# Kernel optimization log

Measured on AMD Instinct MI355X. Metric: run time of the kernel, lower is better.

The kernel has to match this reference:

```python
import jax, jax.numpy as jnp
import numpy as np

B, T, P, D, H = 16, 512, 576, 1024, 16
HD = D // H  # head_dim = 64
SCALE = 1.0 / np.sqrt(HD).astype(np.float32)


def _split_heads(x):
    # [B, S, D] -> [B, H, S, HD]
    b, s, _ = x.shape
    return x.reshape(b, s, H, HD).transpose(0, 2, 1, 3)


def _merge_heads(x):
    # [B, H, S, HD] -> [B, S, D]
    b, h, s, hd = x.shape
    return x.transpose(0, 2, 1, 3).reshape(b, s, h * hd)


def _linear(x, w, b):
    # torch nn.Linear: y = x @ W^T + b, W is [out, in]
    return jnp.einsum('bsd,od->bso', x, w) + b


def setup_inputs() -> dict:
    key = jax.random.key(0)
    ks = jax.random.split(key, 12)
    inp = {
        'text_feats': jax.random.normal(ks[0], (B, T, D), jnp.float32),
        'image_feats': jax.random.normal(ks[1], (B, P, D), jnp.float32),
        'text_mask': jnp.ones((B, T), dtype=bool),
    }
    names = ['qt', 'ki', 'vi', 'qi', 'kt', 'vt', 'ot', 'oi']
    for i, n in enumerate(names):
        inp['w_' + n] = jax.random.normal(ks[2 + i], (D, D), jnp.float32) * 0.02
        inp['b_' + n] = jnp.zeros((D,), jnp.float32)
    return inp


def reference(text_feats, image_feats, text_mask,
              w_qt, b_qt, w_ki, b_ki, w_vi, b_vi,
              w_qi, b_qi, w_kt, b_kt, w_vt, b_vt,
              w_ot, b_ot, w_oi, b_oi):
    # ---- text attends to image (no mask on image keys) ----
    q_t = _split_heads(_linear(text_feats, w_qt, b_qt))    # [B,H,T,HD]
    k_i = _split_heads(_linear(image_feats, w_ki, b_ki))   # [B,H,P,HD]
    v_i = _split_heads(_linear(image_feats, w_vi, b_vi))   # [B,H,P,HD]
    scores_ti = jnp.einsum('bhtd,bhpd->bhtp', q_t, k_i) * SCALE
    attn_ti = jax.nn.softmax(scores_ti, axis=-1)
    text_attended = _merge_heads(jnp.einsum('bhtp,bhpd->bhtd', attn_ti, v_i))
    text_attended = _linear(text_attended, w_ot, b_ot)

    # ---- image attends to text (mask on text keys) ----
    q_i = _split_heads(_linear(image_feats, w_qi, b_qi))   # [B,H,P,HD]
    k_t = _split_heads(_linear(text_feats, w_kt, b_kt))    # [B,H,T,HD]
    v_t = _split_heads(_linear(text_feats, w_vt, b_vt))    # [B,H,T,HD]
    scores_it = jnp.einsum('bhpd,bhtd->bhpt', q_i, k_t) * SCALE
    scores_it = jnp.where(text_mask[:, None, None, :], scores_it, -jnp.inf)
    attn_it = jax.nn.softmax(scores_it, axis=-1)
    image_attended = _merge_heads(jnp.einsum('bhpt,bhtd->bhpd', attn_it, v_t))
    image_attended = _linear(image_attended, w_oi, b_oi)

    return (text_attended, image_attended)
```

## Files before the change

### kernel.cpp

```cpp
#include <hip/hip_runtime.h>
#include <stdint.h>

typedef unsigned short u16;
typedef __bf16 bf16x8 __attribute__((ext_vector_type(8)));
typedef float f32x4 __attribute__((ext_vector_type(4)));

#define SCALE_QK 0.125f

__device__ __forceinline__ u16 f2bf(float f) {
    uint32_t u = __builtin_bit_cast(uint32_t, f);
    u += 0x7FFFu + ((u >> 16) & 1u);
    return (u16)(u >> 16);
}

__device__ __forceinline__ int bdiv(int x, int S) {
    return (S == 512) ? (x >> 9) : (int)(((uint64_t)(x >> 6) * 954437177ull) >> 33);
}

__global__ void cvt_f32_bf16(const float* __restrict__ src, u16* __restrict__ dst, int n4) {
    int i = blockIdx.x * blockDim.x + threadIdx.x;
    if (i >= n4) return;
    float4 v = ((const float4*)src)[i];
    ushort4 o;
    o.x = f2bf(v.x); o.y = f2bf(v.y); o.z = f2bf(v.z); o.w = f2bf(v.w);
    ((ushort4*)dst)[i] = o;
}

__global__ void mask_prep(const int* __restrict__ maski, float* __restrict__ mb, int n) {
    int i = blockIdx.x * blockDim.x + threadIdx.x;
    if (i >= n) return;
    int v0 = maski[0];
    int v = (v0 == 0x01010101) ? (int)((const unsigned char*)maski)[i] : maski[i];
    mb[i] = v ? 0.0f : -1e30f;
}

__device__ __forceinline__ void gload_lds16(const void* g, void* l) {
    __builtin_amdgcn_global_load_lds(
        (__attribute__((address_space(1))) void*)(g),
        (__attribute__((address_space(3))) void*)(l), 16, 0, 0);
}

template<int LAYOUT>
__global__ __launch_bounds__(256)
void gemm_bt(const u16* __restrict__ A, const u16* __restrict__ Bt,
             const float* __restrict__ bias, void* __restrict__ Cout,
             int nx, int K, int ldc, int S, size_t partStride) {
    __shared__ u16 As[128 * 32];
    __shared__ u16 Bs[128 * 32];
    const int tid = threadIdx.x;
    const int wid = tid >> 6, lane = tid & 63;
    const int lo = lane & 15, hi = lane >> 4;
    const int wr = wid >> 1, wc = wid & 1;
    const int id = blockIdx.x;
    const int f = (id & 7) * ((int)gridDim.x >> 3) + (id >> 3);
    const int bm = f / nx, bn = f - bm * nx;
    const u16* Ab = A + (size_t)bm * 128 * K;
    const u16* Bb = Bt + (size_t)bn * 128 * K;
    f32x4 acc[4][4] = {};
    for (int k0 = 0; k0 < K; k0 += 32) {
#pragma unroll
        for (int it = 0; it < 2; ++it) {
            int eo = it * 2048 + wid * 512 + lane * 8;
            int row = eo >> 5, kk = eo & 31;
            gload_lds16(Ab + (size_t)row * K + k0 + kk, As + it * 2048 + wid * 512);
            gload_lds16(Bb + (size_t)row * K + k0 + kk, Bs + it * 2048 + wid * 512);
        }
        __syncthreads();
        bf16x8 af[4], bfr[4];
        const int koff = hi * 8;
#pragma unroll
        for (int m = 0; m < 4; ++m)
            af[m] = *(const bf16x8*)(As + (wr * 64 + m * 16 + lo) * 32 + koff);
#pragma unroll
        for (int n = 0; n < 4; ++n)
            bfr[n] = *(const bf16x8*)(Bs + (wc * 64 + n * 16 + lo) * 32 + koff);
        __builtin_amdgcn_s_setprio(1);
#pragma unroll
        for (int m = 0; m < 4; ++m)
#pragma unroll
            for (int n = 0; n < 4; ++n)
                acc[m][n] = __builtin_amdgcn_mfma_f32_16x16x32_bf16(af[m], bfr[n], acc[m][n], 0, 0, 0);
        __builtin_amdgcn_s_setprio(0);
        __syncthreads();
    }
    const int rowbase = bm * 128 + wr * 64, colbase = bn * 128 + wc * 64;

    if (LAYOUT == 0) {
        float* C = (float*)Cout;
#pragma unroll
        for (int m = 0; m < 4; ++m)
#pragma unroll
            for (int r = 0; r < 4; ++r) {
                int row = rowbase + m * 16 + hi * 4 + r;
#pragma unroll
                for (int n = 0; n < 4; ++n) {
                    int col = colbase + n * 16 + lo;
                    C[(size_t)row * ldc + col] = acc[m][n][r] + bias[col];
                }
            }
    } else if (LAYOUT == 1) {
        const int part = colbase >> 10;
        const int h = (colbase >> 6) & 15;
        u16* base = (u16*)Cout + (size_t)part * partStride;
        float bv[4];
#pragma unroll
        for (int n = 0; n < 4; ++n) bv[n] = bias[colbase + n * 16 + lo];
#pragma unroll
        for (int m = 0; m < 4; ++m)
#pragma unroll
            for (int r = 0; r < 4; ++r) {
                int row = rowbase + m * 16 + hi * 4 + r;
                int b = bdiv(row, S);
                int s = row - b * S;
                u16* rp = base + (((size_t)(b * 16 + h) * S + s) << 6);
#pragma unroll
                for (int n = 0; n < 4; ++n)
                    rp[n * 16 + lo] = f2bf(acc[m][n][r] + bv[n]);
            }
    } else {
        u16* base = (u16*)Cout;
        int bn_[4], s0_[4];
#pragma unroll
        for (int n = 0; n < 4; ++n) {
            int col0 = colbase + n * 16;
            int b = bdiv(col0, S);
            bn_[n] = b;
            s0_[n] = col0 - b * S;
        }
#pragma unroll
        for (int m = 0; m < 4; ++m)
#pragma unroll
            for (int r = 0; r < 4; ++r) {
                int dout = rowbase + m * 16 + hi * 4 + r;
                float bv = bias[dout];
                size_t hd = (size_t)(dout >> 6) * 64 + (dout & 63);
#pragma unroll
                for (int n = 0; n < 4; ++n)
                    base[((size_t)(bn_[n] * 16) * 64 + hd) * S + s0_[n] + lo] =
                        f2bf(acc[m][n][r] + bv);
            }
    }
}

template<int MASKED, int NQ, int SK>
__global__ __launch_bounds__(256)
void attn_v4(const u16* __restrict__ Q, const u16* __restrict__ Kb,
             const u16* __restrict__ Vt, const float* __restrict__ mb,
             u16* __restrict__ Out) {
    constexpr int SQ = NQ * 64;
    constexpr int NC = SK / 64;
    __shared__ u16 kls[2][64 * 64];
    __shared__ u16 vls[2][64 * 64];
    __shared__ u16 pls[4][16 * 72];
    const int tid = threadIdx.x, wid = tid >> 6, lane = tid & 63;
    const int lo = lane & 15, hi = lane >> 4;
    const int id = blockIdx.x;
    const int f = (id & 7) * (NQ * 32) + (id >> 3);
    const int qc = f % NQ, bh = f / NQ;
    const int b = bh >> 4, h = bh & 15;
    const int q0 = qc * 64 + wid * 16;
    const u16* Qp = Q + ((size_t)bh * SQ + q0) * 64;
    const u16* Kp = Kb + (size_t)bh * SK * 64;
    const u16* Vp = Vt + (size_t)bh * 64 * SK;

    bf16x8 qf[2];
#pragma unroll
    for (int ks = 0; ks < 2; ++ks)
        qf[ks] = *(const bf16x8*)(Qp + lo * 64 + ks * 32 + hi * 8);

    f32x4 oacc[4] = {};
    float m = -3e38f, l = 0.f;
    u16* pl = pls[wid];
    uint32_t* pl32 = (uint32_t*)pl;

    auto stage = [&](int bufi, int c0) {
#pragma unroll
        for (int j = 0; j < 2; ++j) {
            const int beta = (j * 4 + wid) * 64 + lane;
            const int row = beta >> 3, slot = beta & 7;
            const int e = (slot ^ (row & 7)) << 3;
            gload_lds16(Kp + (size_t)(c0 + row) * 64 + e,
                        &kls[bufi][0] + (j * 4 + wid) * 512);
            gload_lds16(Vp + (size_t)row * SK + c0 + e,
                        &vls[bufi][0] + (j * 4 + wid) * 512);
        }
    };

    stage(0, 0);
    __syncthreads();

    for (int c = 0; c < NC; ++c) {
        const int c0 = c * 64;
        if (c + 1 < NC) stage((c + 1) & 1, c0 + 64);
        const u16* kb = &kls[c & 1][0];
        const u16* vb = &vls[c & 1][0];

        float sc[4][4];
#pragma unroll
        for (int kt = 0; kt < 4; ++kt) {
            const int krow = kt * 16 + lo;
            const int rx = krow & 7;
            bf16x8 kf0 = *(const bf16x8*)(kb + krow * 64 + ((hi ^ rx) << 3));
            bf16x8 kf1 = *(const bf16x8*)(kb + krow * 64 + (((4 + hi) ^ rx) << 3));
            f32x4 z = {};
            __builtin_amdgcn_s_setprio(1);
            z = __builtin_amdgcn_mfma_f32_16x16x32_bf16(kf0, qf[0], z, 0, 0, 0);
            z = __builtin_amdgcn_mfma_f32_16x16x32_bf16(kf1, qf[1], z, 0, 0, 0);
            __builtin_amdgcn_s_setprio(0);
            if (MASKED) {
                float4 mv = *(const float4*)(mb + b * SK + c0 + kt * 16 + hi * 4);
#pragma unroll
                for (int r = 0; r < 4; ++r) sc[kt][r] = z[r] * SCALE_QK + ((const float*)&mv)[r];
            } else {
#pragma unroll
                for (int r = 0; r < 4; ++r) sc[kt][r] = z[r] * SCALE_QK;
            }
        }
        float a0 = fmaxf(fmaxf(sc[0][0], sc[0][1]), fmaxf(sc[0][2], sc[0][3]));
        float a1 = fmaxf(fmaxf(sc[1][0], sc[1][1]), fmaxf(sc[1][2], sc[1][3]));
        float a2 = fmaxf(fmaxf(sc[2][0], sc[2][1]), fmaxf(sc[2][2], sc[2][3]));
        float a3 = fmaxf(fmaxf(sc[3][0], sc[3][1]), fmaxf(sc[3][2], sc[3][3]));
        float pmax = fmaxf(fmaxf(a0, a1), fmaxf(a2, a3));
        pmax = fmaxf(pmax, __shfl_xor(pmax, 16));
        pmax = fmaxf(pmax, __shfl_xor(pmax, 32));
        if (!__all(pmax - m <= 8.0f)) {
            float mn = fmaxf(m, pmax);
            float alpha = __expf(m - mn);
            m = mn;
            l *= alpha;
#pragma unroll
            for (int n = 0; n < 4; ++n)
#pragma unroll
                for (int r = 0; r < 4; ++r) oacc[n][r] *= alpha;
        }
        float sum = 0.f;
#pragma unroll
        for (int kt = 0; kt < 4; ++kt) {
#pragma unroll
            for (int r = 0; r < 4; ++r) {
                float p = __expf(sc[kt][r] - m);
                sc[kt][r] = p;
                sum += p;
            }
        }
        sum += __shfl_xor(sum, 16);
        sum += __shfl_xor(sum, 32);
        l += sum;
#pragma unroll
        for (int kt = 0; kt < 4; ++kt) {
#pragma unroll
            for (int rp = 0; rp < 2; ++rp) {
                uint32_t w = (uint32_t)f2bf(sc[kt][2 * rp]) |
                             ((uint32_t)f2bf(sc[kt][2 * rp + 1]) << 16);
                pl32[lo * 36 + kt * 8 + hi * 2 + rp] = w;
            }
        }
        bf16x8 pf0 = *(const bf16x8*)(pl + lo * 72 + hi * 8);
        bf16x8 pf1 = *(const bf16x8*)(pl + lo * 72 + 32 + hi * 8);
        __builtin_amdgcn_s_setprio(1);
#pragma unroll
        for (int n = 0; n < 4; ++n) {
            const int d = n * 16 + lo;
            const int dx = d & 7;
            bf16x8 v0 = *(const bf16x8*)(vb + d * 64 + ((hi ^ dx) << 3));
            bf16x8 v1 = *(const bf16x8*)(vb + d * 64 + (((4 + hi) ^ dx) << 3));
            oacc[n] = __builtin_amdgcn_mfma_f32_16x16x32_bf16(v0, pf0, oacc[n], 0, 0, 0);
            oacc[n] = __builtin_amdgcn_mfma_f32_16x16x32_bf16(v1, pf1, oacc[n], 0, 0, 0);
        }
        __builtin_amdgcn_s_setprio(0);
        __syncthreads();
    }
    const float inv = 1.0f / l;
    u16* op = Out + ((size_t)(b * SQ + q0 + lo)) * 1024 + h * 64;
#pragma unroll
    for (int n = 0; n < 4; ++n) {
        ushort4 w;
        w.x = f2bf(oacc[n][0] * inv);
        w.y = f2bf(oacc[n][1] * inv);
        w.z = f2bf(oacc[n][2] * inv);
        w.w = f2bf(oacc[n][3] * inv);
        *(ushort4*)(op + n * 16 + hi * 4) = w;
    }
}

extern "C" void kernel_launch(void* const* d_in, const int* in_sizes, int n_in,
                              void* d_out, int out_size, void* d_ws, size_t ws_size,
                              hipStream_t stream) {
    (void)in_sizes; (void)n_in; (void)out_size; (void)ws_size;
    const float* text  = (const float*)d_in[0];
    const float* image = (const float*)d_in[1];
    const int*   maski = (const int*)d_in[2];
    const float* w_qt = (const float*)d_in[3];  const float* b_qt = (const float*)d_in[4];
    const float* w_ki = (const float*)d_in[5];  const float* b_ki = (const float*)d_in[6];
    const float* w_vi = (const float*)d_in[7];  const float* b_vi = (const float*)d_in[8];
    const float* w_qi = (const float*)d_in[9];  const float* b_qi = (const float*)d_in[10];
    const float* w_kt = (const float*)d_in[11]; const float* b_kt = (const float*)d_in[12];
    const float* w_vt = (const float*)d_in[13]; const float* b_vt = (const float*)d_in[14];
    const float* w_ot = (const float*)d_in[15]; const float* b_ot = (const float*)d_in[16];
    const float* w_oi = (const float*)d_in[17]; const float* b_oi = (const float*)d_in[18];

    const int B = 16, T = 512, P = 576, D = 1024;
    const int MT = B * T;
    const int MI = B * P;

    char* wp = (char*)d_ws;
    auto alloc = [&](size_t bytes) { char* r = wp; wp += (bytes + 255) & ~(size_t)255; return r; };
    u16* Xt    = (u16*)alloc((size_t)MT * D * 2);
    u16* Xi    = (u16*)alloc((size_t)MI * D * 2);
    u16* Wqk_t = (u16*)alloc((size_t)2 * D * D * 2);
    u16* Wqk_i = (u16*)alloc((size_t)2 * D * D * 2);
    u16* Wv_t  = (u16*)alloc((size_t)D * D * 2);
    u16* Wv_i  = (u16*)alloc((size_t)D * D * 2);
    u16* Wot   = (u16*)alloc((size_t)D * D * 2);
    u16* Woi   = (u16*)alloc((size_t)D * D * 2);
    float* bqk_t = (float*)alloc((size_t)2 * D * 4);
    float* bqk_i = (float*)alloc((size_t)2 * D * 4);
    float* mbf   = (float*)alloc((size_t)B * T * 4);
    u16* QKt  = (u16*)alloc((size_t)2 * MT * D * 2);
    u16* QKi  = (u16*)alloc((size_t)2 * MI * D * 2);
    u16* Vtt  = (u16*)alloc((size_t)MT * D * 2);
    u16* Vti  = (u16*)alloc((size_t)MI * D * 2);

    auto cvt = [&](const float* s, u16* d, size_t n) {
        int n4 = (int)(n / 4);
        cvt_f32_bf16<<<(n4 + 255) / 256, 256, 0, stream>>>(s, d, n4);
    };
    cvt(text, Xt, (size_t)MT * D);
    cvt(image, Xi, (size_t)MI * D);
    cvt(w_qt, Wqk_t,                 (size_t)D * D);
    cvt(w_kt, Wqk_t + (size_t)D * D, (size_t)D * D);
    cvt(w_qi, Wqk_i,                 (size_t)D * D);
    cvt(w_ki, Wqk_i + (size_t)D * D, (size_t)D * D);
    cvt(w_vt, Wv_t, (size_t)D * D);
    cvt(w_vi, Wv_i, (size_t)D * D);
    cvt(w_ot, Wot,  (size_t)D * D);
    cvt(w_oi, Woi,  (size_t)D * D);
    hipMemcpyAsync(bqk_t,     b_qt, D * 4, hipMemcpyDeviceToDevice, stream);
    hipMemcpyAsync(bqk_t + D, b_kt, D * 4, hipMemcpyDeviceToDevice, stream);
    hipMemcpyAsync(bqk_i,     b_qi, D * 4, hipMemcpyDeviceToDevice, stream);
    hipMemcpyAsync(bqk_i + D, b_ki, D * 4, hipMemcpyDeviceToDevice, stream);
    mask_prep<<<(B * T + 255) / 256, 256, 0, stream>>>(maski, mbf, B * T);

    gemm_bt<1><<<(2 * D / 128) * (MT / 128), 256, 0, stream>>>(
        Xt, Wqk_t, bqk_t, QKt, 2 * D / 128, D, 0, T, (size_t)MT * D);
    gemm_bt<1><<<(2 * D / 128) * (MI / 128), 256, 0, stream>>>(
        Xi, Wqk_i, bqk_i, QKi, 2 * D / 128, D, 0, P, (size_t)MI * D);
    gemm_bt<2><<<(MT / 128) * (D / 128), 256, 0, stream>>>(
        Wv_t, Xt, b_vt, Vtt, MT / 128, D, 0, T, 0);
    gemm_bt<2><<<(MI / 128) * (D / 128), 256, 0, stream>>>(
        Wv_i, Xi, b_vi, Vti, MI / 128, D, 0, P, 0);

    attn_v4<0, 8, 576><<<8 * 256, 256, 0, stream>>>(
        QKt, QKi + (size_t)MI * D, Vti, nullptr, Xt);
    attn_v4<1, 9, 512><<<9 * 256, 256, 0, stream>>>(
        QKi, QKt + (size_t)MT * D, Vtt, mbf, Xi);

    gemm_bt<0><<<(D / 128) * (MT / 128), 256, 0, stream>>>(
        Xt, Wot, b_ot, d_out, D / 128, D, D, T, 0);
    gemm_bt<0><<<(D / 128) * (MI / 128), 256, 0, stream>>>(
        Xi, Woi, b_oi, (void*)((float*)d_out + (size_t)MT * D), D / 128, D, D, P, 0);
}
```

Measured before the change: 394.7 us.

## Replace GEMMs with 256x256 double-buffered tiles and batch paired launches

```diff
diff --git a/kernel.cpp b/kernel.cpp
--- a/kernel.cpp
+++ b/kernel.cpp
@@ -15,6 +15,12 @@
 
 __device__ __forceinline__ int bdiv(int x, int S) {
     return (S == 512) ? (x >> 9) : (int)(((uint64_t)(x >> 6) * 954437177ull) >> 33);
+}
+
+__device__ __forceinline__ void gload_lds16(const void* g, void* l) {
+    __builtin_amdgcn_global_load_lds(
+        (__attribute__((address_space(1))) void*)(g),
+        (__attribute__((address_space(3))) void*)(l), 16, 0, 0);
 }
 
 __global__ void cvt_f32_bf16(const float* __restrict__ src, u16* __restrict__ dst, int n4) {
@@ -26,99 +32,159 @@
     ((ushort4*)dst)[i] = o;
 }
 
-__global__ void mask_prep(const int* __restrict__ maski, float* __restrict__ mb, int n) {
+struct Ptr8 { const float* p[8]; };
+
+__global__ void cvt_w8(Ptr8 srcs, u16* __restrict__ dst) {
     int i = blockIdx.x * blockDim.x + threadIdx.x;
-    if (i >= n) return;
-    int v0 = maski[0];
-    int v = (v0 == 0x01010101) ? (int)((const unsigned char*)maski)[i] : maski[i];
-    mb[i] = v ? 0.0f : -1e30f;
-}
-
-__device__ __forceinline__ void gload_lds16(const void* g, void* l) {
-    __builtin_amdgcn_global_load_lds(
-        (__attribute__((address_space(1))) void*)(g),
-        (__attribute__((address_space(3))) void*)(l), 16, 0, 0);
+    int mat = i >> 18, off = i & 262143;
+    float4 v = ((const float4*)srcs.p[mat])[off];
+    ushort4 o;
+    o.x = f2bf(v.x); o.y = f2bf(v.y); o.z = f2bf(v.z); o.w = f2bf(v.w);
+    ((ushort4*)(dst + ((size_t)mat << 20)))[off] = o;
+}
+
+__global__ void prep(const int* __restrict__ maski, float* __restrict__ mb,
+                     const float* __restrict__ bqt, const float* __restrict__ bkt,
+                     const float* __restrict__ bqi, const float* __restrict__ bki,
+                     float* __restrict__ biasbuf) {
+    int i = blockIdx.x * blockDim.x + threadIdx.x;
+    if (i < 8192) {
+        int v0 = maski[0];
+        int v = (v0 == 0x01010101) ? (int)((const unsigned char*)maski)[i] : maski[i];
+        mb[i] = v ? 0.0f : -1e30f;
+    } else if (i < 12288) {
+        int j = i - 8192;
+        float v = (j < 1024) ? bqt[j] : (j < 2048) ? bkt[j - 1024]
+                : (j < 3072) ? bqi[j - 2048] : bki[j - 3072];
+        biasbuf[j] = v;
+    }
 }
 
 template<int LAYOUT>
-__global__ __launch_bounds__(256)
-void gemm_bt(const u16* __restrict__ A, const u16* __restrict__ Bt,
-             const float* __restrict__ bias, void* __restrict__ Cout,
-             int nx, int K, int ldc, int S, size_t partStride) {
-    __shared__ u16 As[128 * 32];
-    __shared__ u16 Bs[128 * 32];
+__global__ __launch_bounds__(512)
+void gemm256(const u16* __restrict__ A0, const u16* __restrict__ B0,
+             const float* __restrict__ bias0, void* __restrict__ C0,
+             int nx0, int S0, size_t pstr0, int nblk0,
+             const u16* __restrict__ A1, const u16* __restrict__ B1,
+             const float* __restrict__ bias1, void* __restrict__ C1,
+             int nx1, int S1, size_t pstr1) {
+    constexpr int K = 1024;
+    constexpr int NT = K / 64;
+    __shared__ u16 As[2][256 * 64];
+    __shared__ u16 Bs[2][256 * 64];
     const int tid = threadIdx.x;
     const int wid = tid >> 6, lane = tid & 63;
     const int lo = lane & 15, hi = lane >> 4;
-    const int wr = wid >> 1, wc = wid & 1;
-    const int id = blockIdx.x;
-    const int f = (id & 7) * ((int)gridDim.x >> 3) + (id >> 3);
+    const int wm = wid >> 2, wn = wid & 3;
+    const int tot = (int)gridDim.x;
+    int f = ((int)blockIdx.x & 7) * (tot >> 3) + ((int)blockIdx.x >> 3);
+    const u16 *Ag, *Bg; const float* bias; void* Cg; int nx, S; size_t pstr;
+    if (f < nblk0) { Ag = A0; Bg = B0; bias = bias0; Cg = C0; nx = nx0; S = S0; pstr = pstr0; }
+    else { f -= nblk0; Ag = A1; Bg = B1; bias = bias1; Cg = C1; nx = nx1; S = S1; pstr = pstr1; }
     const int bm = f / nx, bn = f - bm * nx;
-    const u16* Ab = A + (size_t)bm * 128 * K;
-    const u16* Bb = Bt + (size_t)bn * 128 * K;
-    f32x4 acc[4][4] = {};
-    for (int k0 = 0; k0 < K; k0 += 32) {
-#pragma unroll
-        for (int it = 0; it < 2; ++it) {
-            int eo = it * 2048 + wid * 512 + lane * 8;
-            int row = eo >> 5, kk = eo & 31;
-            gload_lds16(Ab + (size_t)row * K + k0 + kk, As + it * 2048 + wid * 512);
-            gload_lds16(Bb + (size_t)row * K + k0 + kk, Bs + it * 2048 + wid * 512);
-        }
-        __syncthreads();
-        bf16x8 af[4], bfr[4];
-        const int koff = hi * 8;
-#pragma unroll
-        for (int m = 0; m < 4; ++m)
-            af[m] = *(const bf16x8*)(As + (wr * 64 + m * 16 + lo) * 32 + koff);
-#pragma unroll
-        for (int n = 0; n < 4; ++n)
-            bfr[n] = *(const bf16x8*)(Bs + (wc * 64 + n * 16 + lo) * 32 + koff);
-        __builtin_amdgcn_s_setprio(1);
-#pragma unroll
-        for (int m = 0; m < 4; ++m)
-#pragma unroll
-            for (int n = 0; n < 4; ++n)
-                acc[m][n] = __builtin_amdgcn_mfma_f32_16x16x32_bf16(af[m], bfr[n], acc[m][n], 0, 0, 0);
-        __builtin_amdgcn_s_setprio(0);
-        __syncthreads();
+    const u16* Ab = Ag + (size_t)bm * 256 * K;
+    const u16* Bb = Bg + (size_t)bn * 256 * K;
+
+    const int srow = tid >> 3;
+    const int sslot = (tid & 7) ^ (srow & 7);
+    const int ldst = (tid >> 6) * 512;
+
+    auto stageA = [&](int buf, int k0, int c) {
+        gload_lds16(Ab + (size_t)(c * 64 + srow) * K + k0 + sslot * 8,
+                    &As[buf][0] + c * 4096 + ldst);
+    };
+    auto stageB = [&](int buf, int k0, int c) {
+        gload_lds16(Bb + (size_t)(c * 64 + srow) * K + k0 + sslot * 8,
+                    &Bs[buf][0] + c * 4096 + ldst);
+    };
+
+    f32x4 acc[8][4] = {};
+
+#pragma unroll
+    for (int c = 0; c < 4; ++c) { stageA(0, 0, c); stageB(0, 0, c); }
+    asm volatile("s_waitcnt vmcnt(0)" ::: "memory");
+    __builtin_amdgcn_s_barrier();
+
+    for (int t = 0; t < NT; ++t) {
+        const int cur = t & 1;
+        const int k0n = (t + 1) * 64;
+        const u16* Atile = &As[cur][0];
+        const u16* Btile = &Bs[cur][0];
+#pragma unroll
+        for (int ph = 0; ph < 4; ++ph) {
+            const int ks = ph >> 1, mh = ph & 1;
+            bf16x8 af[4], bq[4];
+#pragma unroll
+            for (int m = 0; m < 4; ++m) {
+                int row = wm * 128 + mh * 64 + m * 16 + lo;
+                af[m] = *(const bf16x8*)(Atile + row * 64 + (((ks * 4 + hi) ^ (row & 7)) << 3));
+            }
+#pragma unroll
+            for (int n = 0; n < 4; ++n) {
+                int row = wn * 64 + n * 16 + lo;
+                bq[n] = *(const bf16x8*)(Btile + row * 64 + (((ks * 4 + hi) ^ (row & 7)) << 3));
+            }
+            if (t + 1 < NT) {
+                if (ph == 0) {
+#pragma unroll
+                    for (int c = 0; c < 4; ++c) stageA(cur ^ 1, k0n, c);
+                } else if (ph == 1) {
+#pragma unroll
+                    for (int c = 0; c < 4; ++c) stageB(cur ^ 1, k0n, c);
+                }
+            }
+            __builtin_amdgcn_s_barrier();
+            __builtin_amdgcn_s_setprio(1);
+#pragma unroll
+            for (int m = 0; m < 4; ++m)
+#pragma unroll
+                for (int n = 0; n < 4; ++n)
+                    acc[mh * 4 + m][n] =
+                        __builtin_amdgcn_mfma_f32_16x16x32_bf16(af[m], bq[n], acc[mh * 4 + m][n], 0, 0, 0);
+            __builtin_amdgcn_s_setprio(0);
+            if (ph < 3) {
+                __builtin_amdgcn_s_barrier();
+            } else {
+                asm volatile("s_waitcnt vmcnt(0)" ::: "memory");
+                __builtin_amdgcn_s_barrier();
+            }
+        }
     }
-    const int rowbase = bm * 128 + wr * 64, colbase = bn * 128 + wc * 64;
+
+    const int rowbase = bm * 256 + wm * 128, colbase = bn * 256 + wn * 64;
 
     if (LAYOUT == 0) {
-        float* C = (float*)Cout;
-#pragma unroll
-        for (int m = 0; m < 4; ++m)
+        float* C = (float*)Cg;
+#pragma unroll
+        for (int m = 0; m < 8; ++m)
 #pragma unroll
             for (int r = 0; r < 4; ++r) {
                 int row = rowbase + m * 16 + hi * 4 + r;
 #pragma unroll
                 for (int n = 0; n < 4; ++n) {
                     int col = colbase + n * 16 + lo;
-                    C[(size_t)row * ldc + col] = acc[m][n][r] + bias[col];
+                    C[(size_t)row * 1024 + col] = acc[m][n][r] + bias[col];
                 }
             }
     } else if (LAYOUT == 1) {
-        const int part = colbase >> 10;
-        const int h = (colbase >> 6) & 15;
-        u16* base = (u16*)Cout + (size_t)part * partStride;
-        float bv[4];
-#pragma unroll
-        for (int n = 0; n < 4; ++n) bv[n] = bias[colbase + n * 16 + lo];
-#pragma unroll
-        for (int m = 0; m < 4; ++m)
+#pragma unroll
+        for (int m = 0; m < 8; ++m)
 #pragma unroll
             for (int r = 0; r < 4; ++r) {
                 int row = rowbase + m * 16 + hi * 4 + r;
                 int b = bdiv(row, S);
                 int s = row - b * S;
-                u16* rp = base + (((size_t)(b * 16 + h) * S + s) << 6);
-#pragma unroll
-                for (int n = 0; n < 4; ++n)
-                    rp[n * 16 + lo] = f2bf(acc[m][n][r] + bv[n]);
+#pragma unroll
+                for (int n = 0; n < 4; ++n) {
+                    int cb = colbase + n * 16;
+                    int part = cb >> 10, h = (cb >> 6) & 15;
+                    u16* bp = (u16*)Cg + (size_t)part * pstr +
+                              (((size_t)(b * 16 + h) * S + s) << 6) + (cb & 63) + lo;
+                    *bp = f2bf(acc[m][n][r] + bias[cb + lo]);
+                }
             }
     } else {
-        u16* base = (u16*)Cout;
+        u16* base = (u16*)Cg;
         int bn_[4], s0_[4];
 #pragma unroll
         for (int n = 0; n < 4; ++n) {
@@ -128,15 +194,14 @@
             s0_[n] = col0 - b * S;
         }
 #pragma unroll
-        for (int m = 0; m < 4; ++m)
+        for (int m = 0; m < 8; ++m)
 #pragma unroll
             for (int r = 0; r < 4; ++r) {
                 int dout = rowbase + m * 16 + hi * 4 + r;
                 float bv = bias[dout];
-                size_t hd = (size_t)(dout >> 6) * 64 + (dout & 63);
 #pragma unroll
                 for (int n = 0; n < 4; ++n)
-                    base[((size_t)(bn_[n] * 16) * 64 + hd) * S + s0_[n] + lo] =
+                    base[((size_t)bn_[n] * 1024 + dout) * S + s0_[n] + lo] =
                         f2bf(acc[m][n][r] + bv);
             }
     }
@@ -302,61 +367,46 @@
     const int B = 16, T = 512, P = 576, D = 1024;
     const int MT = B * T;
     const int MI = B * P;
+    const size_t M1 = 1 << 20;
 
     char* wp = (char*)d_ws;
     auto alloc = [&](size_t bytes) { char* r = wp; wp += (bytes + 255) & ~(size_t)255; return r; };
-    u16* Xt    = (u16*)alloc((size_t)MT * D * 2);
-    u16* Xi    = (u16*)alloc((size_t)MI * D * 2);
-    u16* Wqk_t = (u16*)alloc((size_t)2 * D * D * 2);
-    u16* Wqk_i = (u16*)alloc((size_t)2 * D * D * 2);
-    u16* Wv_t  = (u16*)alloc((size_t)D * D * 2);
-    u16* Wv_i  = (u16*)alloc((size_t)D * D * 2);
-    u16* Wot   = (u16*)alloc((size_t)D * D * 2);
-    u16* Woi   = (u16*)alloc((size_t)D * D * 2);
-    float* bqk_t = (float*)alloc((size_t)2 * D * 4);
-    float* bqk_i = (float*)alloc((size_t)2 * D * 4);
-    float* mbf   = (float*)alloc((size_t)B * T * 4);
+    u16* Xt   = (u16*)alloc((size_t)MT * D * 2);
+    u16* Xi   = (u16*)alloc((size_t)MI * D * 2);
+    u16* Wall = (u16*)alloc(8 * M1 * 2);
+    float* biasbuf = (float*)alloc(4096 * 4);
+    float* mbf  = (float*)alloc((size_t)B * T * 4);
     u16* QKt  = (u16*)alloc((size_t)2 * MT * D * 2);
     u16* QKi  = (u16*)alloc((size_t)2 * MI * D * 2);
     u16* Vtt  = (u16*)alloc((size_t)MT * D * 2);
     u16* Vti  = (u16*)alloc((size_t)MI * D * 2);
 
-    auto cvt = [&](const float* s, u16* d, size_t n) {
-        int n4 = (int)(n / 4);
-        cvt_f32_bf16<<<(n4 + 255) / 256, 256, 0, stream>>>(s, d, n4);
-    };
-    cvt(text, Xt, (size_t)MT * D);
-    cvt(image, Xi, (size_t)MI * D);
-    cvt(w_qt, Wqk_t,                 (size_t)D * D);
-    cvt(w_kt, Wqk_t + (size_t)D * D, (size_t)D * D);
-    cvt(w_qi, Wqk_i,                 (size_t)D * D);
-    cvt(w_ki, Wqk_i + (size_t)D * D, (size_t)D * D);
-    cvt(w_vt, Wv_t, (size_t)D * D);
-    cvt(w_vi, Wv_i, (size_t)D * D);
-    cvt(w_ot, Wot,  (size_t)D * D);
-    cvt(w_oi, Woi,  (size_t)D * D);
-    hipMemcpyAsync(bqk_t,     b_qt, D * 4, hipMemcpyDeviceToDevice, stream);
-    hipMemcpyAsync(bqk_t + D, b_kt, D * 4, hipMemcpyDeviceToDevice, stream);
-    hipMemcpyAsync(bqk_i,     b_qi, D * 4, hipMemcpyDeviceToDevice, stream);
-    hipMemcpyAsync(bqk_i + D, b_ki, D * 4, hipMemcpyDeviceToDevice, stream);
-    mask_prep<<<(B * T + 255) / 256, 256, 0, stream>>>(maski, mbf, B * T);
-
-    gemm_bt<1><<<(2 * D / 128) * (MT / 128), 256, 0, stream>>>(
-        Xt, Wqk_t, bqk_t, QKt, 2 * D / 128, D, 0, T, (size_t)MT * D);
-    gemm_bt<1><<<(2 * D / 128) * (MI / 128), 256, 0, stream>>>(
-        Xi, Wqk_i, bqk_i, QKi, 2 * D / 128, D, 0, P, (size_t)MI * D);
-    gemm_bt<2><<<(MT / 128) * (D / 128), 256, 0, stream>>>(
-        Wv_t, Xt, b_vt, Vtt, MT / 128, D, 0, T, 0);
-    gemm_bt<2><<<(MI / 128) * (D / 128), 256, 0, stream>>>(
-        Wv_i, Xi, b_vi, Vti, MI / 128, D, 0, P, 0);
+    const u16* Wqk_t = Wall;
+    const u16* Wqk_i = Wall + 2 * M1;
+    const u16* Wv_t  = Wall + 4 * M1;
+    const u16* Wv_i  = Wall + 5 * M1;
+    const u16* Wot   = Wall + 6 * M1;
+    const u16* Woi   = Wall + 7 * M1;
+
+    cvt_f32_bf16<<<(MT * D / 4) / 256, 256, 0, stream>>>(text, Xt, MT * D / 4);
+    cvt_f32_bf16<<<(MI * D / 4) / 256, 256, 0, stream>>>(image, Xi, MI * D / 4);
+    Ptr8 w8 = {{w_qt, w_kt, w_qi, w_ki, w_vt, w_vi, w_ot, w_oi}};
+    cvt_w8<<<8192, 256, 0, stream>>>(w8, Wall);
+    prep<<<48, 256, 0, stream>>>(maski, mbf, b_qt, b_kt, b_qi, b_ki, biasbuf);
+
+    gemm256<1><<<544, 512, 0, stream>>>(
+        Xt, Wqk_t, biasbuf,        QKt, 8, T, (size_t)MT * D, 256,
+        Xi, Wqk_i, biasbuf + 2048, QKi, 8, P, (size_t)MI * D);
+    gemm256<2><<<272, 512, 0, stream>>>(
+        Wv_t, Xt, b_vt, Vtt, 32, T, 0, 128,
+        Wv_i, Xi, b_vi, Vti, 36, P, 0);
 
     attn_v4<0, 8, 576><<<8 * 256, 256, 0, stream>>>(
         QKt, QKi + (size_t)MI * D, Vti, nullptr, Xt);
     attn_v4<1, 9, 512><<<9 * 256, 256, 0, stream>>>(
         QKi, QKt + (size_t)MT * D, Vtt, mbf, Xi);
 
-    gemm_bt<0><<<(D / 128) * (MT / 128), 256, 0, stream>>>(
-        Xt, Wot, b_ot, d_out, D / 128, D, D, T, 0);
-    gemm_bt<0><<<(D / 128) * (MI / 128), 256, 0, stream>>>(
-        Xi, Woi, b_oi, (void*)((float*)d_out + (size_t)MT * D), D / 128, D, D, P, 0);
-}
+    gemm256<0><<<272, 512, 0, stream>>>(
+        Xt, Wot, b_ot, d_out, 4, T, 0, 128,
+        Xi, Woi, b_oi, (void*)((float*)d_out + (size_t)MT * D), 4, P, 0);
+}
```

Measured after the change: 410.5 us. 4.0% more time.
